# Optimization experiments

Measured on AMD Instinct MI355X. Metric: run time of the kernel, lower is better.

Reference implementation:

```python
import jax, jax.numpy as jnp
import numpy as np

N = 40000      # nodes
E = 320000     # edges (avg degree 8)
F_IN = 128     # input channels
H = 4          # attention heads
C = 64         # per-head hidden channels (hidden_features_size entries)
HC = H * C     # 256, width after head concat
OUT = 64       # output classes
BN_EPS = 1e-5
NEG_SLOPE = 0.2


def setup_inputs() -> dict:
    key = jax.random.key(0)
    ks = jax.random.split(key, 16)
    s1 = 1.0 / np.sqrt(F_IN)
    s2 = 1.0 / np.sqrt(HC)
    return {
        "x": jax.random.normal(ks[0], (N, F_IN), jnp.float32),
        "edge_index": jax.random.randint(ks[1], (2, E), 0, N, dtype=jnp.int64),
        "W1": jax.random.normal(ks[2], (F_IN, HC), jnp.float32) * s1,
        "a1_src": jax.random.normal(ks[3], (H, C), jnp.float32) * s2,
        "a1_dst": jax.random.normal(ks[4], (H, C), jnp.float32) * s2,
        "b1": jnp.zeros((HC,), jnp.float32),
        # BatchNorm1d(256)
        "bn1_gamma": jnp.ones((HC,), jnp.float32),
        "bn1_beta": jnp.zeros((HC,), jnp.float32),
        "W2": jax.random.normal(ks[5], (HC, HC), jnp.float32) * s2,
        "a2_src": jax.random.normal(ks[6], (H, C), jnp.float32) * s2,
        "a2_dst": jax.random.normal(ks[7], (H, C), jnp.float32) * s2,
        "b2": jnp.zeros((HC,), jnp.float32),
        # final projection Linear(256 -> 64)
        "linW": jax.random.normal(ks[8], (HC, OUT), jnp.float32) * s2,
        "linb": jnp.zeros((OUT,), jnp.float32),
    }


def gat_conv(x, W, a_src, a_dst, bias, src, dst):
    """PyG GATConv (concat=True, add_self_loops=False, negative_slope=0.2)."""
    h = (x @ W).reshape(-1, H, C)                       # [N,H,C]
    e_src = jnp.einsum("nhc,hc->nh", h, a_src)          # [N,H]
    e_dst = jnp.einsum("nhc,hc->nh", h, a_dst)          # [N,H]
    # per-edge unnormalized attention, message src -> dst
    e = jax.nn.leaky_relu(e_src[src] + e_dst[dst], NEG_SLOPE)   # [E,H]
    # segment softmax over incoming edges of each dst node
    m = jax.ops.segment_max(e, dst, num_segments=N)             # [N,H]
    p = jnp.exp(e - jax.lax.stop_gradient(m)[dst])              # [E,H]
    denom = jax.ops.segment_sum(p, dst, num_segments=N)         # [N,H]
    alpha = p / (denom[dst] + 1e-16)                            # [E,H]
    # weighted scatter-sum aggregation
    out = jax.ops.segment_sum(h[src] * alpha[:, :, None], dst, num_segments=N)  # [N,H,C]
    return out.reshape(-1, HC) + bias


def batch_norm(x, gamma, beta):
    mean = jnp.mean(x, axis=0)
    var = jnp.mean(jnp.square(x - mean), axis=0)
    return (x - mean) * jax.lax.rsqrt(var + BN_EPS) * gamma + beta


def reference(x, edge_index, W1, a1_src, a1_dst, b1, bn1_gamma, bn1_beta,
              W2, a2_src, a2_dst, b2, linW, linb):
    src, dst = edge_index[0], edge_index[1]
    h1 = gat_conv(x, W1, a1_src, a1_dst, b1, src, dst)
    h1 = jax.nn.elu(batch_norm(h1, bn1_gamma, bn1_beta))
    # dropout is identity in eval mode
    h2 = gat_conv(h1, W2, a2_src, a2_dst, b2, src, dst)
    # JumpingKnowledge 'max': elementwise max over layer outputs
    jk = jnp.maximum(h1, h2)
    return jk @ linW + linb
```

## Files before the change

kernel.cpp:

```cpp
#include <hip/hip_runtime.h>
#include <math.h>

#define N_NODES 40000
#define N_EDGES 320000
#define F_IN 128
#define NHEAD 4
#define HC 256
#define NOUT 64

typedef __attribute__((ext_vector_type(8))) __bf16 bf16x8;
typedef __attribute__((ext_vector_type(4))) float f32x4;

static __device__ __forceinline__ unsigned short f2bf(float f) {
    union { float f; unsigned u; } v; v.f = f;
    unsigned r = v.u + 0x7FFFu + ((v.u >> 16) & 1u);
    return (unsigned short)(r >> 16);
}
static __device__ __forceinline__ float bf2f(unsigned short s) {
    union { unsigned u; float f; } v; v.u = ((unsigned)s) << 16;
    return v.f;
}

__global__ __launch_bounds__(256) void prep_kernel(const float* __restrict__ W1,
                                                   const float* __restrict__ W2,
                                                   const float* __restrict__ linW,
                                                   unsigned short* __restrict__ W1t,
                                                   unsigned short* __restrict__ W2t,
                                                   unsigned short* __restrict__ linWt,
                                                   int* __restrict__ zero_ints,
                                                   float* __restrict__ bnacc) {
    int b = blockIdx.x, tid = threadIdx.x;
    if (b < 128) {
        int t = b * 256 + tid;
        int k = t >> 8, n = t & 255;
        W1t[n * 128 + k] = f2bf(W1[t]);
    } else if (b < 384) {
        int t = (b - 128) * 256 + tid;
        int k = t >> 8, n = t & 255;
        W2t[n * 256 + k] = f2bf(W2[t]);
    } else if (b < 448) {
        int t = (b - 384) * 256 + tid;
        int k = t >> 6, n = t & 63;
        linWt[n * 256 + k] = f2bf(linW[t]);
    } else if (b < 527) {
        int i = (b - 448) * 1024 + tid * 4;
        if (i < 80000) *(int4*)(zero_ints + i) = make_int4(0, 0, 0, 0);
    } else {
        if (tid < 512) bnacc[tid] = 0.f;
    }
}

__global__ __launch_bounds__(256) void hist_kernel(const int* __restrict__ ei,
                                                   int* __restrict__ deg) {
    int e = blockIdx.x * 256 + threadIdx.x;
    if (e < N_EDGES) atomicAdd(&deg[ei[N_EDGES + e]], 1);
}

__global__ __launch_bounds__(1024) void scanA_kernel(const int* __restrict__ deg,
                                                     int* __restrict__ rowstart,
                                                     int* __restrict__ blocksum) {
    __shared__ int sm[1024];
    int t = threadIdx.x;
    int i = blockIdx.x * 1024 + t;
    int v = (i < N_NODES) ? deg[i] : 0;
    sm[t] = v;
    __syncthreads();
    for (int off = 1; off < 1024; off <<= 1) {
        int x = (t >= off) ? sm[t - off] : 0;
        __syncthreads();
        sm[t] += x;
        __syncthreads();
    }
    if (i < N_NODES) rowstart[i] = sm[t] - v;
    if (t == 1023) blocksum[blockIdx.x] = sm[1023];
}

__global__ __launch_bounds__(64) void scanB_kernel(int* __restrict__ blocksum,
                                                   int* __restrict__ blockoff) {
    int t = threadIdx.x;
    int v = (t < 40) ? blocksum[t] : 0;
    int s = v;
#pragma unroll
    for (int off = 1; off < 64; off <<= 1) {
        int x = __shfl_up(s, off, 64);
        if (t >= off) s += x;
    }
    if (t < 40) blockoff[t] = s - v;
}

__global__ __launch_bounds__(1024) void scanC_kernel(int* __restrict__ rowstart,
                                                     const int* __restrict__ blockoff) {
    int i = blockIdx.x * 1024 + threadIdx.x;
    if (i < N_NODES) rowstart[i] += blockoff[blockIdx.x];
    if (i == 0) rowstart[N_NODES] = N_EDGES;
}

__global__ __launch_bounds__(256) void scatter_kernel(const int* __restrict__ ei,
                                                      const int* __restrict__ rowstart,
                                                      int* __restrict__ cursor,
                                                      int* __restrict__ esorted) {
    int e = blockIdx.x * 256 + threadIdx.x;
    if (e >= N_EDGES) return;
    int d = ei[N_EDGES + e];
    int s = ei[e];
    int pos = rowstart[d] + atomicAdd(&cursor[d], 1);
    esorted[pos] = s;
}

template <int AMODE>
__global__ __launch_bounds__(256) void gemm_wide(const void* __restrict__ Aptr,
                                                 const unsigned short* __restrict__ Bt,
                                                 const float* __restrict__ sc,
                                                 unsigned short* __restrict__ Cb,
                                                 const float* __restrict__ asrc,
                                                 const float* __restrict__ adst,
                                                 float* __restrict__ es,
                                                 float* __restrict__ ed,
                                                 int K) {
    __shared__ unsigned short As[64 * 32];
    __shared__ unsigned short Bs[256 * 32];
    int tid = threadIdx.x;
    int row0 = blockIdx.x * 64;
    int w = tid >> 6, lane = tid & 63;
    int quad = lane >> 4, l16 = lane & 15;
    f32x4 acc[4][4];
#pragma unroll
    for (int mi = 0; mi < 4; ++mi)
#pragma unroll
        for (int ni = 0; ni < 4; ++ni) acc[mi][ni] = (f32x4){0.f, 0.f, 0.f, 0.f};

    int srow = tid >> 2, schunk = (tid & 3) * 8;
    int brow = tid >> 1, bchunk = (tid & 1) * 16;
    for (int kc = 0; kc < K; kc += 32) {
        if (AMODE == 1) {
            const float* Af = (const float*)Aptr;
            size_t base = (size_t)(row0 + srow) * K + kc + schunk;
            float4 u1 = *(const float4*)(Af + base);
            float4 u2 = *(const float4*)(Af + base + 4);
            ushort4 o1, o2;
            o1.x = f2bf(u1.x); o1.y = f2bf(u1.y); o1.z = f2bf(u1.z); o1.w = f2bf(u1.w);
            o2.x = f2bf(u2.x); o2.y = f2bf(u2.y); o2.z = f2bf(u2.z); o2.w = f2bf(u2.w);
            *(ushort4*)(&As[srow * 32 + schunk]) = o1;
            *(ushort4*)(&As[srow * 32 + schunk + 4]) = o2;
        } else {
            size_t base = (size_t)(row0 + srow) * K + kc + schunk;
            union { int4 v; unsigned short u[8]; } a;
            a.v = *(const int4*)((const unsigned short*)Aptr + base);
            union { int4 v; unsigned short u[8]; } o;
#pragma unroll
            for (int j = 0; j < 8; ++j) {
                int c = kc + schunk + j;
                float v = bf2f(a.u[j]) * sc[c] + sc[HC + c];
                v = v > 0.f ? v : expm1f(v);
                o.u[j] = f2bf(v);
            }
            *(int4*)(&As[srow * 32 + schunk]) = o.v;
        }
#pragma unroll
        for (int p = 0; p < 2; ++p) {
            int n = p * 128 + brow;
            const unsigned short* src = Bt + (size_t)n * K + kc + bchunk;
            *(int4*)(&Bs[n * 32 + bchunk]) = *(const int4*)src;
            *(int4*)(&Bs[n * 32 + bchunk + 8]) = *(const int4*)(src + 8);
        }
        __syncthreads();
        bf16x8 af[4], bfr[4];
#pragma unroll
        for (int mi = 0; mi < 4; ++mi)
            af[mi] = *(const bf16x8*)(&As[(mi * 16 + l16) * 32 + quad * 8]);
#pragma unroll
        for (int ni = 0; ni < 4; ++ni)
            bfr[ni] = *(const bf16x8*)(&Bs[(w * 64 + ni * 16 + l16) * 32 + quad * 8]);
#pragma unroll
        for (int mi = 0; mi < 4; ++mi)
#pragma unroll
            for (int ni = 0; ni < 4; ++ni)
                acc[mi][ni] = __builtin_amdgcn_mfma_f32_16x16x32_bf16(
                    af[mi], bfr[ni], acc[mi][ni], 0, 0, 0);
        __syncthreads();
    }
#pragma unroll
    for (int mi = 0; mi < 4; ++mi)
#pragma unroll
        for (int ni = 0; ni < 4; ++ni) {
            int r0 = row0 + mi * 16 + quad * 4;
            int c = w * 64 + ni * 16 + l16;
#pragma unroll
            for (int r = 0; r < 4; ++r)
                Cb[(size_t)(r0 + r) * HC + c] = f2bf(acc[mi][ni][r]);
        }
    float as_v[4], ad_v[4];
#pragma unroll
    for (int ni = 0; ni < 4; ++ni) {
        int cl = ni * 16 + l16;
        as_v[ni] = asrc[w * 64 + cl];
        ad_v[ni] = adst[w * 64 + cl];
    }
#pragma unroll
    for (int mi = 0; mi < 4; ++mi)
#pragma unroll
        for (int r = 0; r < 4; ++r) {
            float s = 0.f, d = 0.f;
#pragma unroll
            for (int ni = 0; ni < 4; ++ni) {
                s += acc[mi][ni][r] * as_v[ni];
                d += acc[mi][ni][r] * ad_v[ni];
            }
#pragma unroll
            for (int off = 1; off < 16; off <<= 1) {
                s += __shfl_xor(s, off);
                d += __shfl_xor(d, off);
            }
            if (l16 == 0) {
                int row = row0 + mi * 16 + quad * 4 + r;
                es[(size_t)row * NHEAD + w] = s;
                ed[(size_t)row * NHEAD + w] = d;
            }
        }
}

__global__ __launch_bounds__(256) void final_gemm(const unsigned short* __restrict__ A1,
                                                  const unsigned short* __restrict__ A2,
                                                  const unsigned short* __restrict__ Bt,
                                                  const float* __restrict__ sc,
                                                  const float* __restrict__ bias,
                                                  float* __restrict__ Cf) {
    __shared__ unsigned short As[64 * 32];
    __shared__ unsigned short Bs[64 * 32];
    int tid = threadIdx.x;
    int row0 = blockIdx.x * 64;
    int wave = tid >> 6, lane = tid & 63;
    int wm = wave >> 1, wn = wave & 1;
    int quad = lane >> 4, l16 = lane & 15;
    f32x4 acc[2][2];
#pragma unroll
    for (int mi = 0; mi < 2; ++mi)
#pragma unroll
        for (int ni = 0; ni < 2; ++ni) acc[mi][ni] = (f32x4){0.f, 0.f, 0.f, 0.f};

    int srow = tid >> 2, schunk = (tid & 3) * 8;
    for (int kc = 0; kc < HC; kc += 32) {
        {
            size_t base = (size_t)(row0 + srow) * HC + kc + schunk;
            union { int4 v; unsigned short u[8]; } a, b;
            a.v = *(const int4*)(A1 + base);
            b.v = *(const int4*)(A2 + base);
            union { int4 v; unsigned short u[8]; } o;
#pragma unroll
            for (int j = 0; j < 8; ++j) {
                int c = kc + schunk + j;
                float v1 = bf2f(a.u[j]) * sc[c] + sc[HC + c];
                v1 = v1 > 0.f ? v1 : expm1f(v1);
                o.u[j] = f2bf(fmaxf(v1, bf2f(b.u[j])));
            }
            *(int4*)(&As[srow * 32 + schunk]) = o.v;
        }
        {
            int4 bv = *(const int4*)(Bt + (size_t)srow * HC + kc + schunk);
            *(int4*)(&Bs[srow * 32 + schunk]) = bv;
        }
        __syncthreads();
        bf16x8 af[2], bfr[2];
#pragma unroll
        for (int mi = 0; mi < 2; ++mi)
            af[mi] = *(const bf16x8*)(&As[(wm * 32 + mi * 16 + l16) * 32 + quad * 8]);
#pragma unroll
        for (int ni = 0; ni < 2; ++ni)
            bfr[ni] = *(const bf16x8*)(&Bs[(wn * 32 + ni * 16 + l16) * 32 + quad * 8]);
#pragma unroll
        for (int mi = 0; mi < 2; ++mi)
#pragma unroll
            for (int ni = 0; ni < 2; ++ni)
                acc[mi][ni] = __builtin_amdgcn_mfma_f32_16x16x32_bf16(
                    af[mi], bfr[ni], acc[mi][ni], 0, 0, 0);
        __syncthreads();
    }
#pragma unroll
    for (int mi = 0; mi < 2; ++mi)
#pragma unroll
        for (int ni = 0; ni < 2; ++ni) {
            int r0 = row0 + wm * 32 + mi * 16 + quad * 4;
            int c = wn * 32 + ni * 16 + l16;
#pragma unroll
            for (int r = 0; r < 4; ++r)
                Cf[(size_t)(r0 + r) * NOUT + c] = acc[mi][ni][r] + bias[c];
        }
}

__global__ __launch_bounds__(256) void aggregate_kernel(const unsigned short* __restrict__ h,
                                                        const float* __restrict__ es,
                                                        const float* __restrict__ ed,
                                                        const int* __restrict__ rowstart,
                                                        const int* __restrict__ esorted,
                                                        const float* __restrict__ bias,
                                                        unsigned short* __restrict__ outb) {
    int node = blockIdx.x * 4 + (threadIdx.x >> 6);
    int lane = threadIdx.x & 63;
    int hh = lane >> 4;
    float edv = ed[node * NHEAD + hh];
    int beg = rowstart[node], end = rowstart[node + 1];
    float dsum = 0.f;
    float ax = 0.f, ay = 0.f, az = 0.f, aw = 0.f;
    int i = beg;
    for (; i + 8 <= end; i += 8) {
        int s[8];
        ushort4 hv[8];
        float ep[8];
#pragma unroll
        for (int j = 0; j < 8; ++j) s[j] = esorted[i + j];
#pragma unroll
        for (int j = 0; j < 8; ++j)
            hv[j] = *(const ushort4*)(h + (size_t)s[j] * HC + lane * 4);
#pragma unroll
        for (int j = 0; j < 8; ++j) ep[j] = es[s[j] * NHEAD + hh];
#pragma unroll
        for (int j = 0; j < 8; ++j) {
            float e = ep[j] + edv;
            e = e > 0.f ? e : 0.2f * e;
            float w = __expf(e);
            dsum += w;
            ax += w * bf2f(hv[j].x); ay += w * bf2f(hv[j].y);
            az += w * bf2f(hv[j].z); aw += w * bf2f(hv[j].w);
        }
    }
    for (; i + 4 <= end; i += 4) {
        int s[4];
        ushort4 hv[4];
        float ep[4];
#pragma unroll
        for (int j = 0; j < 4; ++j) s[j] = esorted[i + j];
#pragma unroll
        for (int j = 0; j < 4; ++j)
            hv[j] = *(const ushort4*)(h + (size_t)s[j] * HC + lane * 4);
#pragma unroll
        for (int j = 0; j < 4; ++j) ep[j] = es[s[j] * NHEAD + hh];
#pragma unroll
        for (int j = 0; j < 4; ++j) {
            float e = ep[j] + edv;
            e = e > 0.f ? e : 0.2f * e;
            float w = __expf(e);
            dsum += w;
            ax += w * bf2f(hv[j].x); ay += w * bf2f(hv[j].y);
            az += w * bf2f(hv[j].z); aw += w * bf2f(hv[j].w);
        }
    }
    for (; i < end; ++i) {
        int s = esorted[i];
        ushort4 hv = *(const ushort4*)(h + (size_t)s * HC + lane * 4);
        float e = es[s * NHEAD + hh] + edv;
        e = e > 0.f ? e : 0.2f * e;
        float w = __expf(e);
        dsum += w;
        ax += w * bf2f(hv.x); ay += w * bf2f(hv.y);
        az += w * bf2f(hv.z); aw += w * bf2f(hv.w);
    }
    float inv = 1.f / (dsum + 1e-16f);
    float4 bv = *(const float4*)(bias + lane * 4);
    ushort4 o;
    o.x = f2bf(ax * inv + bv.x);
    o.y = f2bf(ay * inv + bv.y);
    o.z = f2bf(az * inv + bv.z);
    o.w = f2bf(aw * inv + bv.w);
    *(ushort4*)(outb + (size_t)node * HC + lane * 4) = o;
}

__global__ __launch_bounds__(256) void bn_stats_kernel(const unsigned short* __restrict__ x,
                                                       float* __restrict__ acc) {
    int c = threadIdx.x;
    int r0 = blockIdx.x * 200;
    float s = 0.f, s2 = 0.f;
    for (int r = r0; r < r0 + 200; ++r) {
        float v = bf2f(x[(size_t)r * HC + c]);
        s += v; s2 += v * v;
    }
    atomicAdd(&acc[c], s);
    atomicAdd(&acc[HC + c], s2);
}

__global__ __launch_bounds__(256) void bn_finalize_kernel(const float* __restrict__ acc,
                                                          const float* __restrict__ gamma,
                                                          const float* __restrict__ beta,
                                                          float* __restrict__ sc) {
    int c = threadIdx.x;
    float mean = acc[c] * (1.f / N_NODES);
    float var = acc[HC + c] * (1.f / N_NODES) - mean * mean;
    float inv = rsqrtf(var + 1e-5f);
    float scale = gamma[c] * inv;
    sc[c] = scale;
    sc[HC + c] = beta[c] - mean * scale;
}

extern "C" void kernel_launch(void* const* d_in, const int* in_sizes, int n_in,
                              void* d_out, int out_size, void* d_ws, size_t ws_size,
                              hipStream_t stream) {
    const float* x      = (const float*)d_in[0];
    const int*   ei     = (const int*)d_in[1];
    const float* W1     = (const float*)d_in[2];
    const float* a1_src = (const float*)d_in[3];
    const float* a1_dst = (const float*)d_in[4];
    const float* b1     = (const float*)d_in[5];
    const float* bn_g   = (const float*)d_in[6];
    const float* bn_b   = (const float*)d_in[7];
    const float* W2     = (const float*)d_in[8];
    const float* a2_src = (const float*)d_in[9];
    const float* a2_dst = (const float*)d_in[10];
    const float* b2     = (const float*)d_in[11];
    const float* linW   = (const float*)d_in[12];
    const float* linb   = (const float*)d_in[13];
    float* out = (float*)d_out;

    char* ws = (char*)d_ws;
    const size_t NHC_BF = (size_t)N_NODES * HC * 2;
    unsigned short* hpre_b  = (unsigned short*)(ws);
    unsigned short* h1agg_b = (unsigned short*)(ws + NHC_BF);
    unsigned short* h2_b    = (unsigned short*)(ws + 2 * NHC_BF);
    char* p = ws + 3 * NHC_BF;
    unsigned short* W1t   = (unsigned short*)p; p += (size_t)F_IN * HC * 2;
    unsigned short* W2t   = (unsigned short*)p; p += (size_t)HC * HC * 2;
    unsigned short* linWt = (unsigned short*)p; p += (size_t)HC * NOUT * 2;
    float* e_src   = (float*)p;  p += (size_t)N_NODES * NHEAD * 4;
    float* e_dst   = (float*)p;  p += (size_t)N_NODES * NHEAD * 4;
    int*   deg     = (int*)p;    p += (size_t)N_NODES * 4;
    int*   cursor  = (int*)p;    p += (size_t)N_NODES * 4;
    int*   rowstart= (int*)p;    p += ((size_t)N_NODES + 64) * 4;
    int*   esorted = (int*)p;    p += (size_t)N_EDGES * 4;
    int*   blocksum= (int*)p;    p += 64 * 4;
    int*   blockoff= (int*)p;    p += 64 * 4;
    float* bnacc   = (float*)p;  p += 2 * HC * 4;
    float* bnsc    = (float*)p;  p += 2 * HC * 4;

    prep_kernel<<<528, 256, 0, stream>>>(W1, W2, linW, W1t, W2t, linWt, deg, bnacc);

    hist_kernel<<<(N_EDGES + 255) / 256, 256, 0, stream>>>(ei, deg);
    scanA_kernel<<<40, 1024, 0, stream>>>(deg, rowstart, blocksum);
    scanB_kernel<<<1, 64, 0, stream>>>(blocksum, blockoff);
    scanC_kernel<<<40, 1024, 0, stream>>>(rowstart, blockoff);
    scatter_kernel<<<(N_EDGES + 255) / 256, 256, 0, stream>>>(ei, rowstart, cursor, esorted);

    gemm_wide<1><<<N_NODES / 64, 256, 0, stream>>>(
        x, W1t, nullptr, hpre_b, a1_src, a1_dst, e_src, e_dst, F_IN);
    aggregate_kernel<<<N_NODES / 4, 256, 0, stream>>>(hpre_b, e_src, e_dst, rowstart,
                                                      esorted, b1, h1agg_b);
    bn_stats_kernel<<<N_NODES / 200, 256, 0, stream>>>(h1agg_b, bnacc);
    bn_finalize_kernel<<<1, 256, 0, stream>>>(bnacc, bn_g, bn_b, bnsc);

    gemm_wide<3><<<N_NODES / 64, 256, 0, stream>>>(
        h1agg_b, W2t, bnsc, hpre_b, a2_src, a2_dst, e_src, e_dst, HC);
    aggregate_kernel<<<N_NODES / 4, 256, 0, stream>>>(hpre_b, e_src, e_dst, rowstart,
                                                      esorted, b2, h2_b);

    final_gemm<<<N_NODES / 64, 256, 0, stream>>>(h1agg_b, h2_b, linWt, bnsc, linb, out);
}
```

Before: 271.6 us.

## Fold scan block-offset and BN finalize into consumer kernels to cut launches

```diff
diff --git a/kernel.cpp b/kernel.cpp
--- a/kernel.cpp
+++ b/kernel.cpp
@@ -7,6 +7,7 @@
 #define NHEAD 4
 #define HC 256
 #define NOUT 64
+#define NSCANB 40
 
 typedef __attribute__((ext_vector_type(8))) __bf16 bf16x8;
 typedef __attribute__((ext_vector_type(4))) float f32x4;
@@ -19,6 +20,21 @@
 static __device__ __forceinline__ float bf2f(unsigned short s) {
     union { unsigned u; float f; } v; v.u = ((unsigned)s) << 16;
     return v.f;
+}
+
+static __device__ __forceinline__ void scan_blockoff(const int* __restrict__ blocksum,
+                                                     int* loff, int tid) {
+    if (tid < 64) {
+        int v = (tid < NSCANB) ? blocksum[tid] : 0;
+        int s = v;
+#pragma unroll
+        for (int off = 1; off < 64; off <<= 1) {
+            int x = __shfl_up(s, off, 64);
+            if (tid >= off) s += x;
+        }
+        if (tid < NSCANB) loff[tid] = s - v;
+    }
+    __syncthreads();
 }
 
 __global__ __launch_bounds__(256) void prep_kernel(const float* __restrict__ W1,
@@ -44,7 +60,7 @@
         linWt[n * 256 + k] = f2bf(linW[t]);
     } else if (b < 527) {
         int i = (b - 448) * 1024 + tid * 4;
-        if (i < 80000) *(int4*)(zero_ints + i) = make_int4(0, 0, 0, 0);
+        if (i < 80004) *(int4*)(zero_ints + i) = make_int4(0, 0, 0, 0);
     } else {
         if (tid < 512) bnacc[tid] = 0.f;
     }
@@ -75,35 +91,19 @@
     if (t == 1023) blocksum[blockIdx.x] = sm[1023];
 }
 
-__global__ __launch_bounds__(64) void scanB_kernel(int* __restrict__ blocksum,
-                                                   int* __restrict__ blockoff) {
-    int t = threadIdx.x;
-    int v = (t < 40) ? blocksum[t] : 0;
-    int s = v;
-#pragma unroll
-    for (int off = 1; off < 64; off <<= 1) {
-        int x = __shfl_up(s, off, 64);
-        if (t >= off) s += x;
-    }
-    if (t < 40) blockoff[t] = s - v;
-}
-
-__global__ __launch_bounds__(1024) void scanC_kernel(int* __restrict__ rowstart,
-                                                     const int* __restrict__ blockoff) {
-    int i = blockIdx.x * 1024 + threadIdx.x;
-    if (i < N_NODES) rowstart[i] += blockoff[blockIdx.x];
-    if (i == 0) rowstart[N_NODES] = N_EDGES;
-}
-
 __global__ __launch_bounds__(256) void scatter_kernel(const int* __restrict__ ei,
                                                       const int* __restrict__ rowstart,
+                                                      const int* __restrict__ blocksum,
                                                       int* __restrict__ cursor,
                                                       int* __restrict__ esorted) {
-    int e = blockIdx.x * 256 + threadIdx.x;
+    __shared__ int loff[NSCANB];
+    int tid = threadIdx.x;
+    scan_blockoff(blocksum, loff, tid);
+    int e = blockIdx.x * 256 + tid;
     if (e >= N_EDGES) return;
     int d = ei[N_EDGES + e];
     int s = ei[e];
-    int pos = rowstart[d] + atomicAdd(&cursor[d], 1);
+    int pos = rowstart[d] + loff[d >> 10] + atomicAdd(&cursor[d], 1);
     esorted[pos] = s;
 }
 
@@ -291,23 +291,29 @@
                                                         const float* __restrict__ es,
                                                         const float* __restrict__ ed,
                                                         const int* __restrict__ rowstart,
+                                                        const int* __restrict__ blocksum,
                                                         const int* __restrict__ esorted,
                                                         const float* __restrict__ bias,
                                                         unsigned short* __restrict__ outb) {
-    int node = blockIdx.x * 4 + (threadIdx.x >> 6);
-    int lane = threadIdx.x & 63;
+    __shared__ int loff[NSCANB];
+    int tid = threadIdx.x;
+    scan_blockoff(blocksum, loff, tid);
+    int node = blockIdx.x * 4 + (tid >> 6);
+    int lane = tid & 63;
     int hh = lane >> 4;
     float edv = ed[node * NHEAD + hh];
-    int beg = rowstart[node], end = rowstart[node + 1];
+    int beg = rowstart[node] + loff[node >> 10];
+    int end = (node + 1 == N_NODES) ? N_EDGES
+                                    : rowstart[node + 1] + loff[(node + 1) >> 10];
     float dsum = 0.f;
     float ax = 0.f, ay = 0.f, az = 0.f, aw = 0.f;
-    int i = beg;
-    for (; i + 8 <= end; i += 8) {
+    for (int i = beg; i < end; i += 8) {
+        int cnt = end - i;
         int s[8];
         ushort4 hv[8];
         float ep[8];
 #pragma unroll
-        for (int j = 0; j < 8; ++j) s[j] = esorted[i + j];
+        for (int j = 0; j < 8; ++j) s[j] = esorted[min(i + j, end - 1)];
 #pragma unroll
         for (int j = 0; j < 8; ++j)
             hv[j] = *(const ushort4*)(h + (size_t)s[j] * HC + lane * 4);
@@ -318,41 +324,11 @@
             float e = ep[j] + edv;
             e = e > 0.f ? e : 0.2f * e;
             float w = __expf(e);
+            w = (j < cnt) ? w : 0.f;
             dsum += w;
             ax += w * bf2f(hv[j].x); ay += w * bf2f(hv[j].y);
             az += w * bf2f(hv[j].z); aw += w * bf2f(hv[j].w);
         }
-    }
-    for (; i + 4 <= end; i += 4) {
-        int s[4];
-        ushort4 hv[4];
-        float ep[4];
-#pragma unroll
-        for (int j = 0; j < 4; ++j) s[j] = esorted[i + j];
-#pragma unroll
-        for (int j = 0; j < 4; ++j)
-            hv[j] = *(const ushort4*)(h + (size_t)s[j] * HC + lane * 4);
-#pragma unroll
-        for (int j = 0; j < 4; ++j) ep[j] = es[s[j] * NHEAD + hh];
-#pragma unroll
-        for (int j = 0; j < 4; ++j) {
-            float e = ep[j] + edv;
-            e = e > 0.f ? e : 0.2f * e;
-            float w = __expf(e);
-            dsum += w;
-            ax += w * bf2f(hv[j].x); ay += w * bf2f(hv[j].y);
-            az += w * bf2f(hv[j].z); aw += w * bf2f(hv[j].w);
-        }
-    }
-    for (; i < end; ++i) {
-        int s = esorted[i];
-        ushort4 hv = *(const ushort4*)(h + (size_t)s * HC + lane * 4);
-        float e = es[s * NHEAD + hh] + edv;
-        e = e > 0.f ? e : 0.2f * e;
-        float w = __expf(e);
-        dsum += w;
-        ax += w * bf2f(hv.x); ay += w * bf2f(hv.y);
-        az += w * bf2f(hv.z); aw += w * bf2f(hv.w);
     }
     float inv = 1.f / (dsum + 1e-16f);
     float4 bv = *(const float4*)(bias + lane * 4);
@@ -365,7 +341,11 @@
 }
 
 __global__ __launch_bounds__(256) void bn_stats_kernel(const unsigned short* __restrict__ x,
-                                                       float* __restrict__ acc) {
+                                                       float* __restrict__ acc,
+                                                       const float* __restrict__ gamma,
+                                                       const float* __restrict__ beta,
+                                                       float* __restrict__ sc,
+                                                       int* __restrict__ ticket) {
     int c = threadIdx.x;
     int r0 = blockIdx.x * 200;
     float s = 0.f, s2 = 0.f;
@@ -375,19 +355,21 @@
     }
     atomicAdd(&acc[c], s);
     atomicAdd(&acc[HC + c], s2);
-}
-
-__global__ __launch_bounds__(256) void bn_finalize_kernel(const float* __restrict__ acc,
-                                                          const float* __restrict__ gamma,
-                                                          const float* __restrict__ beta,
-                                                          float* __restrict__ sc) {
-    int c = threadIdx.x;
-    float mean = acc[c] * (1.f / N_NODES);
-    float var = acc[HC + c] * (1.f / N_NODES) - mean * mean;
-    float inv = rsqrtf(var + 1e-5f);
-    float scale = gamma[c] * inv;
-    sc[c] = scale;
-    sc[HC + c] = beta[c] - mean * scale;
+    __threadfence();
+    __syncthreads();
+    __shared__ int is_last;
+    if (c == 0) is_last = (atomicAdd(ticket, 1) == (int)gridDim.x - 1);
+    __syncthreads();
+    if (is_last) {
+        float sum = atomicAdd(&acc[c], 0.f);
+        float sq  = atomicAdd(&acc[HC + c], 0.f);
+        float mean = sum * (1.f / N_NODES);
+        float var = sq * (1.f / N_NODES) - mean * mean;
+        float inv = rsqrtf(var + 1e-5f);
+        float scale = gamma[c] * inv;
+        sc[c] = scale;
+        sc[HC + c] = beta[c] - mean * scale;
+    }
 }
 
 extern "C" void kernel_launch(void* const* d_in, const int* in_sizes, int n_in,
@@ -422,10 +404,10 @@
     float* e_dst   = (float*)p;  p += (size_t)N_NODES * NHEAD * 4;
     int*   deg     = (int*)p;    p += (size_t)N_NODES * 4;
     int*   cursor  = (int*)p;    p += (size_t)N_NODES * 4;
+    int*   ticket  = (int*)p;    p += 4 * 4;
     int*   rowstart= (int*)p;    p += ((size_t)N_NODES + 64) * 4;
     int*   esorted = (int*)p;    p += (size_t)N_EDGES * 4;
     int*   blocksum= (int*)p;    p += 64 * 4;
-    int*   blockoff= (int*)p;    p += 64 * 4;
     float* bnacc   = (float*)p;  p += 2 * HC * 4;
     float* bnsc    = (float*)p;  p += 2 * HC * 4;
 
@@ -433,21 +415,20 @@
 
     hist_kernel<<<(N_EDGES + 255) / 256, 256, 0, stream>>>(ei, deg);
     scanA_kernel<<<40, 1024, 0, stream>>>(deg, rowstart, blocksum);
-    scanB_kernel<<<1, 64, 0, stream>>>(blocksum, blockoff);
-    scanC_kernel<<<40, 1024, 0, stream>>>(rowstart, blockoff);
-    scatter_kernel<<<(N_EDGES + 255) / 256, 256, 0, stream>>>(ei, rowstart, cursor, esorted);
+    scatter_kernel<<<(N_EDGES + 255) / 256, 256, 0, stream>>>(ei, rowstart, blocksum,
+                                                              cursor, esorted);
 
     gemm_wide<1><<<N_NODES / 64, 256, 0, stream>>>(
         x, W1t, nullptr, hpre_b, a1_src, a1_dst, e_src, e_dst, F_IN);
     aggregate_kernel<<<N_NODES / 4, 256, 0, stream>>>(hpre_b, e_src, e_dst, rowstart,
-                                                      esorted, b1, h1agg_b);
-    bn_stats_kernel<<<N_NODES / 200, 256, 0, stream>>>(h1agg_b, bnacc);
-    bn_finalize_kernel<<<1, 256, 0, stream>>>(bnacc, bn_g, bn_b, bnsc);
+                                                      blocksum, esorted, b1, h1agg_b);
+    bn_stats_kernel<<<N_NODES / 200, 256, 0, stream>>>(h1agg_b, bnacc, bn_g, bn_b,
+                                                       bnsc, ticket);
 
     gemm_wide<3><<<N_NODES / 64, 256, 0, stream>>>(
         h1agg_b, W2t, bnsc, hpre_b, a2_src, a2_dst, e_src, e_dst, HC);
     aggregate_kernel<<<N_NODES / 4, 256, 0, stream>>>(hpre_b, e_src, e_dst, rowstart,
-                                                      esorted, b2, h2_b);
+                                                      blocksum, esorted, b2, h2_b);
 
     final_gemm<<<N_NODES / 64, 256, 0, stream>>>(h1agg_b, h2_b, linWt, bnsc, linb, out);
 }
```

New measurement: 284.1 us. 4.6% more time.

## Prefetch GEMM tiles into registers and fuse JK max into layer-2 aggregation

Applied to the files above, without the earlier changes.

```diff
diff --git a/kernel.cpp b/kernel.cpp
--- a/kernel.cpp
+++ b/kernel.cpp
@@ -111,6 +111,7 @@
 __global__ __launch_bounds__(256) void gemm_wide(const void* __restrict__ Aptr,
                                                  const unsigned short* __restrict__ Bt,
                                                  const float* __restrict__ sc,
+                                                 unsigned short* __restrict__ h1p,
                                                  unsigned short* __restrict__ Cb,
                                                  const float* __restrict__ asrc,
                                                  const float* __restrict__ adst,
@@ -131,38 +132,67 @@
 
     int srow = tid >> 2, schunk = (tid & 3) * 8;
     int brow = tid >> 1, bchunk = (tid & 1) * 16;
+
+    float4 pa0, pa1;
+    int4 pai;
+    int4 pb[4];
+    if (AMODE == 1) {
+        const float* Af = (const float*)Aptr;
+        size_t base = (size_t)(row0 + srow) * K + schunk;
+        pa0 = *(const float4*)(Af + base);
+        pa1 = *(const float4*)(Af + base + 4);
+    } else {
+        pai = *(const int4*)((const unsigned short*)Aptr + (size_t)(row0 + srow) * K + schunk);
+    }
+    {
+        const unsigned short* s0 = Bt + (size_t)brow * K + bchunk;
+        const unsigned short* s1 = Bt + (size_t)(128 + brow) * K + bchunk;
+        pb[0] = *(const int4*)s0; pb[1] = *(const int4*)(s0 + 8);
+        pb[2] = *(const int4*)s1; pb[3] = *(const int4*)(s1 + 8);
+    }
+
     for (int kc = 0; kc < K; kc += 32) {
+        union { int4 v; unsigned short u[8]; } aS;
         if (AMODE == 1) {
-            const float* Af = (const float*)Aptr;
-            size_t base = (size_t)(row0 + srow) * K + kc + schunk;
-            float4 u1 = *(const float4*)(Af + base);
-            float4 u2 = *(const float4*)(Af + base + 4);
-            ushort4 o1, o2;
-            o1.x = f2bf(u1.x); o1.y = f2bf(u1.y); o1.z = f2bf(u1.z); o1.w = f2bf(u1.w);
-            o2.x = f2bf(u2.x); o2.y = f2bf(u2.y); o2.z = f2bf(u2.z); o2.w = f2bf(u2.w);
-            *(ushort4*)(&As[srow * 32 + schunk]) = o1;
-            *(ushort4*)(&As[srow * 32 + schunk + 4]) = o2;
+            aS.u[0] = f2bf(pa0.x); aS.u[1] = f2bf(pa0.y);
+            aS.u[2] = f2bf(pa0.z); aS.u[3] = f2bf(pa0.w);
+            aS.u[4] = f2bf(pa1.x); aS.u[5] = f2bf(pa1.y);
+            aS.u[6] = f2bf(pa1.z); aS.u[7] = f2bf(pa1.w);
         } else {
-            size_t base = (size_t)(row0 + srow) * K + kc + schunk;
             union { int4 v; unsigned short u[8]; } a;
-            a.v = *(const int4*)((const unsigned short*)Aptr + base);
-            union { int4 v; unsigned short u[8]; } o;
+            a.v = pai;
 #pragma unroll
             for (int j = 0; j < 8; ++j) {
                 int c = kc + schunk + j;
                 float v = bf2f(a.u[j]) * sc[c] + sc[HC + c];
                 v = v > 0.f ? v : expm1f(v);
-                o.u[j] = f2bf(v);
+                aS.u[j] = f2bf(v);
             }
-            *(int4*)(&As[srow * 32 + schunk]) = o.v;
-        }
-#pragma unroll
-        for (int p = 0; p < 2; ++p) {
-            int n = p * 128 + brow;
-            const unsigned short* src = Bt + (size_t)n * K + kc + bchunk;
-            *(int4*)(&Bs[n * 32 + bchunk]) = *(const int4*)src;
-            *(int4*)(&Bs[n * 32 + bchunk + 8]) = *(const int4*)(src + 8);
-        }
+        }
+        int4 bS0 = pb[0], bS1 = pb[1], bS2 = pb[2], bS3 = pb[3];
+        int kn = kc + 32;
+        if (kn < K) {
+            if (AMODE == 1) {
+                const float* Af = (const float*)Aptr;
+                size_t base = (size_t)(row0 + srow) * K + kn + schunk;
+                pa0 = *(const float4*)(Af + base);
+                pa1 = *(const float4*)(Af + base + 4);
+            } else {
+                pai = *(const int4*)((const unsigned short*)Aptr +
+                                     (size_t)(row0 + srow) * K + kn + schunk);
+            }
+            const unsigned short* s0 = Bt + (size_t)brow * K + kn + bchunk;
+            const unsigned short* s1 = Bt + (size_t)(128 + brow) * K + kn + bchunk;
+            pb[0] = *(const int4*)s0; pb[1] = *(const int4*)(s0 + 8);
+            pb[2] = *(const int4*)s1; pb[3] = *(const int4*)(s1 + 8);
+        }
+        *(int4*)(&As[srow * 32 + schunk]) = aS.v;
+        if (AMODE == 3)
+            *(int4*)(h1p + (size_t)(row0 + srow) * HC + kc + schunk) = aS.v;
+        *(int4*)(&Bs[brow * 32 + bchunk]) = bS0;
+        *(int4*)(&Bs[brow * 32 + bchunk + 8]) = bS1;
+        *(int4*)(&Bs[(128 + brow) * 32 + bchunk]) = bS2;
+        *(int4*)(&Bs[(128 + brow) * 32 + bchunk + 8]) = bS3;
         __syncthreads();
         bf16x8 af[4], bfr[4];
 #pragma unroll
@@ -219,10 +249,8 @@
         }
 }
 
-__global__ __launch_bounds__(256) void final_gemm(const unsigned short* __restrict__ A1,
-                                                  const unsigned short* __restrict__ A2,
+__global__ __launch_bounds__(256) void final_gemm(const unsigned short* __restrict__ A,
                                                   const unsigned short* __restrict__ Bt,
-                                                  const float* __restrict__ sc,
                                                   const float* __restrict__ bias,
                                                   float* __restrict__ Cf) {
     __shared__ unsigned short As[64 * 32];
@@ -239,26 +267,18 @@
         for (int ni = 0; ni < 2; ++ni) acc[mi][ni] = (f32x4){0.f, 0.f, 0.f, 0.f};
 
     int srow = tid >> 2, schunk = (tid & 3) * 8;
+    int4 pa = *(const int4*)(A + (size_t)(row0 + srow) * HC + schunk);
+    int4 pbv = *(const int4*)(Bt + (size_t)srow * HC + schunk);
+
     for (int kc = 0; kc < HC; kc += 32) {
-        {
-            size_t base = (size_t)(row0 + srow) * HC + kc + schunk;
-            union { int4 v; unsigned short u[8]; } a, b;
-            a.v = *(const int4*)(A1 + base);
-            b.v = *(const int4*)(A2 + base);
-            union { int4 v; unsigned short u[8]; } o;
-#pragma unroll
-            for (int j = 0; j < 8; ++j) {
-                int c = kc + schunk + j;
-                float v1 = bf2f(a.u[j]) * sc[c] + sc[HC + c];
-                v1 = v1 > 0.f ? v1 : expm1f(v1);
-                o.u[j] = f2bf(fmaxf(v1, bf2f(b.u[j])));
-            }
-            *(int4*)(&As[srow * 32 + schunk]) = o.v;
-        }
-        {
-            int4 bv = *(const int4*)(Bt + (size_t)srow * HC + kc + schunk);
-            *(int4*)(&Bs[srow * 32 + schunk]) = bv;
-        }
+        int4 aS = pa, bS = pbv;
+        int kn = kc + 32;
+        if (kn < HC) {
+            pa = *(const int4*)(A + (size_t)(row0 + srow) * HC + kn + schunk);
+            pbv = *(const int4*)(Bt + (size_t)srow * HC + kn + schunk);
+        }
+        *(int4*)(&As[srow * 32 + schunk]) = aS;
+        *(int4*)(&Bs[srow * 32 + schunk]) = bS;
         __syncthreads();
         bf16x8 af[2], bfr[2];
 #pragma unroll
@@ -287,12 +307,14 @@
         }
 }
 
+template <int JK>
 __global__ __launch_bounds__(256) void aggregate_kernel(const unsigned short* __restrict__ h,
                                                         const float* __restrict__ es,
                                                         const float* __restrict__ ed,
                                                         const int* __restrict__ rowstart,
                                                         const int* __restrict__ esorted,
                                                         const float* __restrict__ bias,
+                                                        const unsigned short* __restrict__ h1p,
                                                         unsigned short* __restrict__ outb) {
     int node = blockIdx.x * 4 + (threadIdx.x >> 6);
     int lane = threadIdx.x & 63;
@@ -357,10 +379,18 @@
     float inv = 1.f / (dsum + 1e-16f);
     float4 bv = *(const float4*)(bias + lane * 4);
     ushort4 o;
-    o.x = f2bf(ax * inv + bv.x);
-    o.y = f2bf(ay * inv + bv.y);
-    o.z = f2bf(az * inv + bv.z);
-    o.w = f2bf(aw * inv + bv.w);
+    if (JK == 0) {
+        o.x = f2bf(ax * inv + bv.x);
+        o.y = f2bf(ay * inv + bv.y);
+        o.z = f2bf(az * inv + bv.z);
+        o.w = f2bf(aw * inv + bv.w);
+    } else {
+        ushort4 h1v = *(const ushort4*)(h1p + (size_t)node * HC + lane * 4);
+        o.x = f2bf(fmaxf(bf2f(h1v.x), ax * inv + bv.x));
+        o.y = f2bf(fmaxf(bf2f(h1v.y), ay * inv + bv.y));
+        o.z = f2bf(fmaxf(bf2f(h1v.z), az * inv + bv.z));
+        o.w = f2bf(fmaxf(bf2f(h1v.w), aw * inv + bv.w));
+    }
     *(ushort4*)(outb + (size_t)node * HC + lane * 4) = o;
 }
 
@@ -413,8 +443,9 @@
     const size_t NHC_BF = (size_t)N_NODES * HC * 2;
     unsigned short* hpre_b  = (unsigned short*)(ws);
     unsigned short* h1agg_b = (unsigned short*)(ws + NHC_BF);
-    unsigned short* h2_b    = (unsigned short*)(ws + 2 * NHC_BF);
-    char* p = ws + 3 * NHC_BF;
+    unsigned short* h1p_b   = (unsigned short*)(ws + 2 * NHC_BF);
+    unsigned short* jk_b    = (unsigned short*)(ws + 3 * NHC_BF);
+    char* p = ws + 4 * NHC_BF;
     unsigned short* W1t   = (unsigned short*)p; p += (size_t)F_IN * HC * 2;
     unsigned short* W2t   = (unsigned short*)p; p += (size_t)HC * HC * 2;
     unsigned short* linWt = (unsigned short*)p; p += (size_t)HC * NOUT * 2;
@@ -438,16 +469,16 @@
     scatter_kernel<<<(N_EDGES + 255) / 256, 256, 0, stream>>>(ei, rowstart, cursor, esorted);
 
     gemm_wide<1><<<N_NODES / 64, 256, 0, stream>>>(
-        x, W1t, nullptr, hpre_b, a1_src, a1_dst, e_src, e_dst, F_IN);
-    aggregate_kernel<<<N_NODES / 4, 256, 0, stream>>>(hpre_b, e_src, e_dst, rowstart,
-                                                      esorted, b1, h1agg_b);
+        x, W1t, nullptr, nullptr, hpre_b, a1_src, a1_dst, e_src, e_dst, F_IN);
+    aggregate_kernel<0><<<N_NODES / 4, 256, 0, stream>>>(
+        hpre_b, e_src, e_dst, rowstart, esorted, b1, nullptr, h1agg_b);
     bn_stats_kernel<<<N_NODES / 200, 256, 0, stream>>>(h1agg_b, bnacc);
     bn_finalize_kernel<<<1, 256, 0, stream>>>(bnacc, bn_g, bn_b, bnsc);
 
     gemm_wide<3><<<N_NODES / 64, 256, 0, stream>>>(
-        h1agg_b, W2t, bnsc, hpre_b, a2_src, a2_dst, e_src, e_dst, HC);
-    aggregate_kernel<<<N_NODES / 4, 256, 0, stream>>>(hpre_b, e_src, e_dst, rowstart,
-                                                      esorted, b2, h2_b);
-
-    final_gemm<<<N_NODES / 64, 256, 0, stream>>>(h1agg_b, h2_b, linWt, bnsc, linb, out);
-}
+        h1agg_b, W2t, bnsc, h1p_b, hpre_b, a2_src, a2_dst, e_src, e_dst, HC);
+    aggregate_kernel<1><<<N_NODES / 4, 256, 0, stream>>>(
+        hpre_b, e_src, e_dst, rowstart, esorted, b2, h1p_b, jk_b);
+
+    final_gemm<<<N_NODES / 64, 256, 0, stream>>>(jk_b, linWt, linb, out);
+}
```

Result: faster. 260.6 us (-4.0%).
